# Optimization experiments

Hardware: AMD Instinct MI355X
Metric: run time of the kernel (lower is better)

## Reference

```python
import jax, jax.numpy as jnp
import numpy as np

B, T, D_IN, D, KS = 8, 2048, 64, 512, 3
N_LAYERS = 6
TOP_P = 0.25


def _causal_conv(x, w, b, dil):
    # x: [B, C_in, T], w: [C_out, C_in, K] -> [B, C_out, T]
    pad = (w.shape[-1] - 1) * dil
    y = jax.lax.conv_general_dilated(
        x, w, window_strides=(1,), padding=[(pad, 0)], rhs_dilation=(dil,),
        dimension_numbers=('NCH', 'OIH', 'NCH'))
    return y + b[None, :, None]


def setup_inputs() -> dict:
    key = jax.random.key(0)
    ks = jax.random.split(key, 20)
    s = 0.02
    inp = {
        'x': jax.random.normal(ks[0], (B, T, D_IN), jnp.float32),
        # block 0 (d_in=64 -> d_model=512, dilation 1) + 1x1 residual
        'c1w0': jax.random.normal(ks[1], (D, D_IN, KS), jnp.float32) * s,
        'c1b0': jnp.zeros((D,), jnp.float32),
        'c2w0': jax.random.normal(ks[2], (D, D, KS), jnp.float32) * s,
        'c2b0': jnp.zeros((D,), jnp.float32),
        'resw': jax.random.normal(ks[3], (D, D_IN, 1), jnp.float32) * s,
        'resb': jnp.zeros((D,), jnp.float32),
        # blocks 1..5 stacked (512 -> 512, dilations 2,4,8,16,32), identity residual
        'c1w': jax.random.normal(ks[4], (N_LAYERS - 1, D, D, KS), jnp.float32) * s,
        'c1b': jnp.zeros((N_LAYERS - 1, D), jnp.float32),
        'c2w': jax.random.normal(ks[5], (N_LAYERS - 1, D, D, KS), jnp.float32) * s,
        'c2b': jnp.zeros((N_LAYERS - 1, D), jnp.float32),
        # attention projections (torch Linear: y = x @ W.T + b, W [out,in])
        'wq': jax.random.normal(ks[6], (D, D), jnp.float32) * s,
        'bq': jnp.zeros((D,), jnp.float32),
        'wk': jax.random.normal(ks[7], (D, D), jnp.float32) * s,
        'bk': jnp.zeros((D,), jnp.float32),
        'wv': jax.random.normal(ks[8], (D, D), jnp.float32) * s,
        'bv': jnp.zeros((D,), jnp.float32),
        'wp': jax.random.normal(ks[9], (D, D), jnp.float32) * s,
        'bp': jnp.zeros((D,), jnp.float32),
    }
    return inp


def _forward(x, c1w0, c1b0, c2w0, c2b0, resw, resb, c1w, c1b, c2w, c2b,
             wq, bq, wk, bk, wv, bv, wp, bp):
    gelu = lambda t: jax.nn.gelu(t, approximate=False)
    h = jnp.swapaxes(x, 1, 2)  # [B, D_IN, T]
    # block 0 with 1x1-conv residual (d_in != d_out)
    y = gelu(_causal_conv(h, c1w0, c1b0, 1))
    y = gelu(_causal_conv(y, c2w0, c2b0, 1))
    h = y + _causal_conv(h, resw, resb, 1)
    # blocks 1..5, identity residual
    for i in range(N_LAYERS - 1):
        dil = 2 ** (i + 1)
        y = gelu(_causal_conv(h, c1w[i], c1b[i], dil))
        y = gelu(_causal_conv(y, c2w[i], c2b[i], dil))
        h = y + h
    z = jnp.swapaxes(h, 1, 2)  # [B, T, D]

    # sparse top-p attention
    q = z @ wq.T + bq
    k = z @ wk.T + bk
    v = z @ wv.T + bv
    scores = jnp.einsum('bqd,bkd->bqk', q, k) / jnp.sqrt(jnp.float32(D))
    k_keep = max(1, int(TOP_P * T))
    vals, idx = jax.lax.top_k(scores, k_keep)  # [B, T, k_keep]
    neg_inf = jnp.array(-jnp.inf, scores.dtype)
    mask = jnp.full_like(scores, neg_inf)
    b_ix = jnp.arange(B)[:, None, None]
    t_ix = jnp.arange(T)[None, :, None]
    mask = mask.at[b_ix, t_ix, idx].set(vals)
    attn = jax.nn.softmax(mask, axis=-1)
    attn_out = jnp.einsum('bqk,bkd->bqd', attn, v)[:, -1, :]  # [B, D]

    return (z[:, -1, :] + attn_out) @ wp.T + bp


def reference(x, c1w0, c1b0, c2w0, c2b0, resw, resb, c1w, c1b, c2w, c2b,
              wq, bq, wk, bk, wv, bv, wp, bp):
    return _forward(x, c1w0, c1b0, c2w0, c2b0, resw, resb, c1w, c1b, c2w, c2b,
                    wq, bq, wk, bk, wv, bv, wp, bp)
```

## Files before the change

kernel.cpp:

```cpp
#include <hip/hip_runtime.h>
#include <hip/hip_bf16.h>
#include <math.h>

#define B_ 8
#define T_ 2048
#define PT_ 2112
#define DIN_ 64
#define D_ 512

typedef __attribute__((ext_vector_type(8))) short bf16x8;
typedef __attribute__((ext_vector_type(4))) float f32x4;

#define HROW(b, t) (((size_t)(b) * PT_ + 64 + (t)) * D_)

__device__ __forceinline__ float gelu_f(float x) {
    return 0.5f * x * (1.0f + erff(x * 0.70710678118654752440f));
}
__device__ __forceinline__ float bfu2f(unsigned short u) {
    union { float f; unsigned int i; } v; v.i = ((unsigned int)u) << 16; return v.f;
}
__device__ __forceinline__ unsigned short f2bf(float f) {
    unsigned int x = __float_as_uint(f);
    return (unsigned short)((x + 0x7FFFu + ((x >> 16) & 1u)) >> 16);
}
__device__ __forceinline__ void gload_lds16(const void* g, void* l) {
    __builtin_amdgcn_global_load_lds(
        (const __attribute__((address_space(1))) void*)g,
        (__attribute__((address_space(3))) void*)l, 16, 0, 0);
}

__global__ __launch_bounds__(256) void k_zeropad(unsigned short* xb,
                                                 unsigned short* bufA,
                                                 unsigned short* bufB) {
    const int NX = B_ * 64 * DIN_;
    const int NA = B_ * 64 * D_;
    int i = blockIdx.x * 256 + threadIdx.x;
    if (i < NX) {
        const int b = i / (64 * DIN_), r = i - b * (64 * DIN_);
        xb[(size_t)b * PT_ * DIN_ + r] = 0;
        return;
    }
    i -= NX;
    if (i < NA) {
        const int b = i / (64 * D_), r = i - b * (64 * D_);
        bufA[(size_t)b * PT_ * D_ + r] = 0;
        return;
    }
    i -= NA;
    if (i < NA) {
        const int b = i / (64 * D_), r = i - b * (64 * D_);
        bufB[(size_t)b * PT_ * D_ + r] = 0;
    }
}

__global__ __launch_bounds__(256) void k_xcvt(const float* __restrict__ x,
                                              unsigned short* __restrict__ xb, int n) {
    const int i = blockIdx.x * 256 + threadIdx.x;
    if (i >= n) return;
    const int b = i / (T_ * DIN_);
    const int r = i - b * (T_ * DIN_);
    xb[((size_t)b * PT_ + 64) * DIN_ + r] = f2bf(x[i]);
}

__global__ __launch_bounds__(256) void k_wcvt(const float* __restrict__ src,
                                              unsigned short* __restrict__ dst,
                                              int C_in, int KS) {
    const int n = 512 * C_in * KS;
    const size_t base = (size_t)blockIdx.y * n;
    for (int i = blockIdx.x * 256 + threadIdx.x; i < n; i += gridDim.x * 256) {
        const int ci = i % C_in;
        const int r = i / C_in;
        const int co = r & 511;
        const int tap = r >> 9;
        dst[base + i] = f2bf(src[base + ((size_t)co * C_in + ci) * KS + tap]);
    }
}

template <int KS, int MODE>
__global__ __launch_bounds__(256, 2) void k_conv_mfma(const unsigned short* __restrict__ X,
                                                      const unsigned short* __restrict__ Wt,
                                                      const float* __restrict__ bias,
                                                      const unsigned short* R,
                                                      unsigned short* Y,
                                                      int C_in, int dil) {
    constexpr int XROWS = 192;
    constexpr int WROWS = KS * 128;
    constexpr int WSLOTS = WROWS * 8;

    const int tid = threadIdx.x;
    const int t0 = blockIdx.x * 128;
    const int co0 = blockIdx.y * 128;
    const int b = blockIdx.z;
    const int back = (KS - 1) * dil;

    __shared__ __align__(16) unsigned short sX[XROWS * 64];
    __shared__ __align__(16) unsigned short sW[WROWS * 64];

    const int lane = tid & 63;
    const int wv = tid >> 6;
    const int wco = (wv & 1) * 64;
    const int wt = (wv >> 1) * 64;
    const int tl = lane & 15;
    const int ch = lane >> 4;

    f32x4 acc[4][4] = {};

    const unsigned short* Xb = X + ((size_t)b * PT_ + 64) * C_in;

    const unsigned short* xsrc[6];
#pragma unroll
    for (int k = 0; k < 6; ++k) {
        const int i = tid + k * 256;
        const int row = i >> 3, s = i & 7;
        int tg = t0 - back + row;
        if (tg >= T_) tg = T_ - 1;
        xsrc[k] = Xb + (size_t)tg * C_in + ((s ^ (row & 7)) << 3);
    }
    const unsigned short* wsrc[WSLOTS / 256];
#pragma unroll
    for (int k = 0; k < WSLOTS / 256; ++k) {
        const int i = tid + k * 256;
        const int row = i >> 3, s = i & 7;
        const int tap = row >> 7, rco = row & 127;
        wsrc[k] = Wt + ((size_t)(tap * 512 + co0 + rco)) * C_in + ((s ^ (row & 7)) << 3);
    }

    const int NC = C_in >> 6;
    for (int c = 0; c < NC; ++c) {
        if (c) __syncthreads();
#pragma unroll
        for (int k = 0; k < 6; ++k) {
            const int i = tid + k * 256;
            gload_lds16(xsrc[k], &sX[(i & ~63) * 8]);
            xsrc[k] += 64;
        }
#pragma unroll
        for (int k = 0; k < WSLOTS / 256; ++k) {
            const int i = tid + k * 256;
            gload_lds16(wsrc[k], &sW[(i & ~63) * 8]);
            wsrc[k] += 64;
        }
        __syncthreads();

#pragma unroll
        for (int tap = 0; tap < KS; ++tap) {
            const int tapoff = tap * dil;
#pragma unroll
            for (int ks = 0; ks < 2; ++ks) {
                const int j = ks * 4 + ch;
                bf16x8 a[4], bb[4];
#pragma unroll
                for (int m = 0; m < 4; ++m) {
                    const int wr = tap * 128 + wco + m * 16 + tl;
                    a[m] = *reinterpret_cast<const bf16x8*>(
                        &sW[wr * 64 + ((j ^ (wr & 7)) << 3)]);
                }
#pragma unroll
                for (int n = 0; n < 4; ++n) {
                    const int xr = wt + n * 16 + tl + tapoff;
                    bb[n] = *reinterpret_cast<const bf16x8*>(
                        &sX[xr * 64 + ((j ^ (xr & 7)) << 3)]);
                }
#pragma unroll
                for (int m = 0; m < 4; ++m)
#pragma unroll
                    for (int n = 0; n < 4; ++n)
                        acc[m][n] = __builtin_amdgcn_mfma_f32_16x16x32_bf16(a[m], bb[n], acc[m][n], 0, 0, 0);
            }
        }
    }

#pragma unroll
    for (int m = 0; m < 4; ++m) {
        const int co = co0 + wco + m * 16 + ch * 4;
        const float4 bv4 = *reinterpret_cast<const float4*>(&bias[co]);
#pragma unroll
        for (int n = 0; n < 4; ++n) {
            const int t = t0 + wt + n * 16 + tl;
            const size_t base = HROW(b, t) + co;
            float v[4];
            v[0] = acc[m][n][0] + bv4.x;
            v[1] = acc[m][n][1] + bv4.y;
            v[2] = acc[m][n][2] + bv4.z;
            v[3] = acc[m][n][3] + bv4.w;
            if (MODE >= 1) {
#pragma unroll
                for (int r = 0; r < 4; ++r) v[r] = gelu_f(v[r]);
            }
            if (MODE == 2) {
                const uint2 rr = *reinterpret_cast<const uint2*>(&R[base]);
                v[0] += bfu2f((unsigned short)(rr.x & 0xffffu));
                v[1] += bfu2f((unsigned short)(rr.x >> 16));
                v[2] += bfu2f((unsigned short)(rr.y & 0xffffu));
                v[3] += bfu2f((unsigned short)(rr.y >> 16));
            }
            uint2 o;
            o.x = (unsigned int)f2bf(v[0]) | ((unsigned int)f2bf(v[1]) << 16);
            o.y = (unsigned int)f2bf(v[2]) | ((unsigned int)f2bf(v[3]) << 16);
            *reinterpret_cast<uint2*>(&Y[base]) = o;
        }
    }
}

__global__ __launch_bounds__(256) void k_q(const unsigned short* __restrict__ h,
                                           const float* __restrict__ wq,
                                           const float* __restrict__ bq,
                                           float* __restrict__ q) {
    __shared__ float zs[B_ * D_];
    const int tid = threadIdx.x;
    for (int i = tid; i < B_ * D_; i += 256) {
        const int b = i >> 9, c = i & 511;
        zs[i] = bfu2f(h[HROW(b, T_ - 1) + c]);
    }
    __syncthreads();
    const int wvi = tid >> 6, lane = tid & 63;
    const int d = blockIdx.x * 4 + wvi;
    const float* wr = wq + (size_t)d * D_ + lane * 8;
    float w8[8];
#pragma unroll
    for (int j = 0; j < 8; ++j) w8[j] = wr[j];
    float acc[B_];
#pragma unroll
    for (int b = 0; b < B_; ++b) {
        float a = 0.0f;
#pragma unroll
        for (int j = 0; j < 8; ++j) a += w8[j] * zs[b * D_ + lane * 8 + j];
        acc[b] = a;
    }
#pragma unroll
    for (int off = 32; off; off >>= 1) {
#pragma unroll
        for (int b = 0; b < B_; ++b) acc[b] += __shfl_xor(acc[b], off);
    }
    if (lane == 0) {
#pragma unroll
        for (int b = 0; b < B_; ++b) q[b * D_ + d] = acc[b] + bq[d];
    }
}

__global__ __launch_bounds__(512) void k_qk(const float* __restrict__ q,
                                            const float* __restrict__ wk,
                                            const float* __restrict__ bk,
                                            float* __restrict__ qkvec,
                                            float* __restrict__ qbk) {
    const int b = blockIdx.y, dc = blockIdx.x;
    const int tid = threadIdx.x;
    __shared__ float qs[64];
    if (tid < 64) qs[tid] = q[b * D_ + dc * 64 + tid];
    __syncthreads();
    float acc = 0.0f;
    const float* wbase = wk + (size_t)(dc * 64) * D_ + tid;
#pragma unroll 8
    for (int d = 0; d < 64; ++d) acc += qs[d] * wbase[(size_t)d * D_];
    atomicAdd(&qkvec[b * D_ + tid], acc);
    if (tid < 64) {
        float p = qs[tid] * bk[dc * 64 + tid];
#pragma unroll
        for (int off = 32; off; off >>= 1) p += __shfl_xor(p, off);
        if (tid == 0) atomicAdd(&qbk[b], p);
    }
}

__global__ __launch_bounds__(256) void k_scores(const unsigned short* __restrict__ h,
                                                const float* __restrict__ qkvec,
                                                const float* __restrict__ qbk,
                                                float* __restrict__ scores) {
    const int b = blockIdx.y;
    const int tid = threadIdx.x;
    __shared__ float qs[D_];
    qs[tid] = qkvec[b * D_ + tid];
    qs[tid + 256] = qkvec[b * D_ + tid + 256];
    __syncthreads();
    const int wvi = tid >> 6, lane = tid & 63;
    const int t = blockIdx.x * 4 + wvi;
    const uint4 v = *reinterpret_cast<const uint4*>(h + HROW(b, t) + lane * 8);
    const unsigned int w[4] = {v.x, v.y, v.z, v.w};
    float acc = 0.0f;
#pragma unroll
    for (int j = 0; j < 4; ++j) {
        acc += bfu2f((unsigned short)(w[j] & 0xffffu)) * qs[lane * 8 + 2 * j];
        acc += bfu2f((unsigned short)(w[j] >> 16)) * qs[lane * 8 + 2 * j + 1];
    }
    for (int off = 32; off; off >>= 1) acc += __shfl_down(acc, off);
    if (lane == 0) scores[b * T_ + t] = (acc + qbk[b]) * 0.04419417382415922f;
}

__global__ __launch_bounds__(1024) void k_topk(const float* __restrict__ scores,
                                               float* __restrict__ wts) {
    const int b = blockIdx.x;
    __shared__ float s[T_];
    __shared__ float v[T_];
    __shared__ float red[16];
    __shared__ float denom_s;
    for (int i = threadIdx.x; i < T_; i += 1024) {
        const float x = scores[b * T_ + i];
        s[i] = x; v[i] = x;
    }
    __syncthreads();
    for (unsigned kk = 2; kk <= T_; kk <<= 1) {
        for (unsigned j = kk >> 1; j > 0; j >>= 1) {
            for (unsigned i = threadIdx.x; i < T_; i += 1024) {
                const unsigned ixj = i ^ j;
                if (ixj > i) {
                    const float a = v[i], c2 = v[ixj];
                    const bool asc = ((i & kk) == 0);
                    if ((a > c2) == asc) { v[i] = c2; v[ixj] = a; }
                }
            }
            __syncthreads();
        }
    }
    const float thr = v[T_ - 512];
    const float mx = v[T_ - 1];
    float part = 0.0f;
    for (int i = threadIdx.x; i < T_; i += 1024) {
        const float x = s[i];
        if (x >= thr) part += expf(x - mx);
    }
    for (int off = 32; off; off >>= 1) part += __shfl_down(part, off);
    const int lane = threadIdx.x & 63, wv_ = threadIdx.x >> 6;
    if (lane == 0) red[wv_] = part;
    __syncthreads();
    if (threadIdx.x == 0) {
        float d = 0.0f;
        for (int i = 0; i < 16; ++i) d += red[i];
        denom_s = d;
    }
    __syncthreads();
    const float inv = 1.0f / denom_s;
    for (int i = threadIdx.x; i < T_; i += 1024) {
        const float x = s[i];
        wts[b * T_ + i] = (x >= thr) ? expf(x - mx) * inv : 0.0f;
    }
}

__global__ __launch_bounds__(256) void k_zv(const unsigned short* __restrict__ h,
                                            const float* __restrict__ wts,
                                            float* __restrict__ zvb) {
    const int b = blockIdx.y;
    const int t0 = blockIdx.x * 256;
    const int tid = threadIdx.x;
    float a0 = 0.0f, a1 = 0.0f;
    for (int t = t0; t < t0 + 256; ++t) {
        const float w = wts[b * T_ + t];
        if (w != 0.0f) {
            const unsigned int v = *reinterpret_cast<const unsigned int*>(
                h + HROW(b, t) + tid * 2);
            a0 += w * bfu2f((unsigned short)(v & 0xffffu));
            a1 += w * bfu2f((unsigned short)(v >> 16));
        }
    }
    atomicAdd(&zvb[b * D_ + tid * 2], a0);
    atomicAdd(&zvb[b * D_ + tid * 2 + 1], a1);
}

__global__ __launch_bounds__(256) void k_u(const unsigned short* __restrict__ h,
                                           const float* __restrict__ zvb,
                                           const float* __restrict__ wv,
                                           const float* __restrict__ bv,
                                           float* __restrict__ u) {
    __shared__ float zs[B_ * D_];
    const int tid = threadIdx.x;
    for (int i = tid; i < B_ * D_; i += 256) zs[i] = zvb[i];
    __syncthreads();
    const int wvi = tid >> 6, lane = tid & 63;
    const int e = blockIdx.x * 4 + wvi;
    const float* wr = wv + (size_t)e * D_ + lane * 8;
    float w8[8];
#pragma unroll
    for (int j = 0; j < 8; ++j) w8[j] = wr[j];
    float acc[B_];
#pragma unroll
    for (int b = 0; b < B_; ++b) {
        float a = 0.0f;
#pragma unroll
        for (int j = 0; j < 8; ++j) a += w8[j] * zs[b * D_ + lane * 8 + j];
        acc[b] = a;
    }
#pragma unroll
    for (int off = 32; off; off >>= 1) {
#pragma unroll
        for (int b = 0; b < B_; ++b) acc[b] += __shfl_xor(acc[b], off);
    }
    if (lane == 0) {
#pragma unroll
        for (int b = 0; b < B_; ++b)
            u[b * D_ + e] = acc[b] + bv[e] + bfu2f(h[HROW(b, T_ - 1) + e]);
    }
}

__global__ __launch_bounds__(256) void k_out(const float* __restrict__ u,
                                             const float* __restrict__ wp,
                                             const float* __restrict__ bp,
                                             float* __restrict__ out) {
    __shared__ float us[B_ * D_];
    const int tid = threadIdx.x;
    for (int i = tid; i < B_ * D_; i += 256) us[i] = u[i];
    __syncthreads();
    const int wvi = tid >> 6, lane = tid & 63;
    const int d = blockIdx.x * 4 + wvi;
    const float* wr = wp + (size_t)d * D_ + lane * 8;
    float w8[8];
#pragma unroll
    for (int j = 0; j < 8; ++j) w8[j] = wr[j];
    float acc[B_];
#pragma unroll
    for (int b = 0; b < B_; ++b) {
        float a = 0.0f;
#pragma unroll
        for (int j = 0; j < 8; ++j) a += w8[j] * us[b * D_ + lane * 8 + j];
        acc[b] = a;
    }
#pragma unroll
    for (int off = 32; off; off >>= 1) {
#pragma unroll
        for (int b = 0; b < B_; ++b) acc[b] += __shfl_xor(acc[b], off);
    }
    if (lane == 0) {
#pragma unroll
        for (int b = 0; b < B_; ++b) out[b * D_ + d] = acc[b] + bp[d];
    }
}

extern "C" void kernel_launch(void* const* d_in, const int* in_sizes, int n_in,
                              void* d_out, int out_size, void* d_ws, size_t ws_size,
                              hipStream_t stream) {
    const float* x    = (const float*)d_in[0];
    const float* c1w0 = (const float*)d_in[1];
    const float* c1b0 = (const float*)d_in[2];
    const float* c2w0 = (const float*)d_in[3];
    const float* c2b0 = (const float*)d_in[4];
    const float* resw = (const float*)d_in[5];
    const float* resb = (const float*)d_in[6];
    const float* c1w  = (const float*)d_in[7];
    const float* c1b  = (const float*)d_in[8];
    const float* c2w  = (const float*)d_in[9];
    const float* c2b  = (const float*)d_in[10];
    const float* wq   = (const float*)d_in[11];
    const float* bq   = (const float*)d_in[12];
    const float* wk   = (const float*)d_in[13];
    const float* bk   = (const float*)d_in[14];
    const float* wvp  = (const float*)d_in[15];
    const float* bv   = (const float*)d_in[16];
    const float* wp   = (const float*)d_in[17];
    const float* bp   = (const float*)d_in[18];
    float* out = (float*)d_out;

    unsigned short* ws16 = (unsigned short*)d_ws;
    unsigned short* xb   = ws16;
    unsigned short* bufA = xb + (size_t)B_ * PT_ * DIN_;
    unsigned short* bufB = bufA + (size_t)B_ * PT_ * D_;
    unsigned short* wRes = bufB + (size_t)B_ * PT_ * D_;
    unsigned short* wC10 = wRes + 512 * 64;
    unsigned short* wC20 = wC10 + 3 * 512 * 64;
    unsigned short* wC1  = wC20 + 3 * 512 * 512;
    unsigned short* wC2  = wC1 + (size_t)5 * 3 * 512 * 512;
    float* fws  = (float*)(wC2 + (size_t)5 * 3 * 512 * 512);
    float* qv    = fws;
    float* qkvec = qv + B_ * D_;
    float* qbk   = qkvec + B_ * D_;
    float* zvb   = qbk + 8;
    float* uacc  = zvb + B_ * D_;
    float* sc    = uacc + B_ * D_;
    float* wts   = sc + B_ * T_;

    k_zeropad<<<dim3((B_ * 64 * (DIN_ + 2 * D_) + 255) / 256), 256, 0, stream>>>(xb, bufA, bufB);
    k_xcvt<<<dim3((B_ * T_ * DIN_ + 255) / 256), 256, 0, stream>>>(x, xb, B_ * T_ * DIN_);
    k_wcvt<<<dim3(128, 1), 256, 0, stream>>>(resw, wRes, DIN_, 1);
    k_wcvt<<<dim3(384, 1), 256, 0, stream>>>(c1w0, wC10, DIN_, 3);
    k_wcvt<<<dim3(768, 1), 256, 0, stream>>>(c2w0, wC20, D_, 3);
    k_wcvt<<<dim3(768, 5), 256, 0, stream>>>(c1w, wC1, D_, 3);
    k_wcvt<<<dim3(768, 5), 256, 0, stream>>>(c2w, wC2, D_, 3);
    hipMemsetAsync(qkvec, 0, (2 * B_ * D_ + 8) * sizeof(float), stream);

    const dim3 cgrid(T_ / 128, D_ / 128, B_);
    k_conv_mfma<1, 0><<<cgrid, 256, 0, stream>>>(xb, wRes, resb, nullptr, bufA, DIN_, 1);
    k_conv_mfma<3, 1><<<cgrid, 256, 0, stream>>>(xb, wC10, c1b0, nullptr, bufB, DIN_, 1);
    k_conv_mfma<3, 2><<<cgrid, 256, 0, stream>>>(bufB, wC20, c2b0, bufA, bufA, D_, 1);
    for (int i = 0; i < 5; ++i) {
        const int dil = 2 << i;
        k_conv_mfma<3, 1><<<cgrid, 256, 0, stream>>>(bufA, wC1 + (size_t)i * 3 * 512 * 512,
                                                     c1b + i * D_, nullptr, bufB, D_, dil);
        k_conv_mfma<3, 2><<<cgrid, 256, 0, stream>>>(bufB, wC2 + (size_t)i * 3 * 512 * 512,
                                                     c2b + i * D_, bufA, bufA, D_, dil);
    }

    k_q<<<128, 256, 0, stream>>>(bufA, wq, bq, qv);
    k_qk<<<dim3(8, 8), 512, 0, stream>>>(qv, wk, bk, qkvec, qbk);
    k_scores<<<dim3(T_ / 4, B_), 256, 0, stream>>>(bufA, qkvec, qbk, sc);
    k_topk<<<B_, 1024, 0, stream>>>(sc, wts);
    k_zv<<<dim3(T_ / 256, B_), 256, 0, stream>>>(bufA, wts, zvb);
    k_u<<<128, 256, 0, stream>>>(bufA, zvb, wvp, bv, uacc);
    k_out<<<128, 256, 0, stream>>>(uacc, wp, bp, out);
}
```

Before: 475.0 us.

## Software-pipeline conv MFMA kernel with double-buffered per-tap weight and input staging

Restructures the conv main loop into per-tap phases with double-buffered LDS for both inputs and weights. Global-to-LDS loads for the next tap or channel chunk are issued before the current MFMAs, with explicit vmcnt/lgkmcnt waits and barriers. MFMA blocks are wrapped in s_setprio to favour compute issue. The aim is to hide global load latency behind matrix math, at the cost of more barriers and fragile hand-tuned wait counts.

Result: slower. 491.3 us (+3.4%).

```diff
diff --git a/kernel.cpp b/kernel.cpp
--- a/kernel.cpp
+++ b/kernel.cpp
@@ -83,18 +83,14 @@
                                                       const unsigned short* R,
                                                       unsigned short* Y,
                                                       int C_in, int dil) {
-    constexpr int XROWS = 192;
-    constexpr int WROWS = KS * 128;
-    constexpr int WSLOTS = WROWS * 8;
-
     const int tid = threadIdx.x;
     const int t0 = blockIdx.x * 128;
     const int co0 = blockIdx.y * 128;
     const int b = blockIdx.z;
     const int back = (KS - 1) * dil;
 
-    __shared__ __align__(16) unsigned short sX[XROWS * 64];
-    __shared__ __align__(16) unsigned short sW[WROWS * 64];
+    __shared__ __align__(16) unsigned short sX[2][192 * 64];
+    __shared__ __align__(16) unsigned short sW[2][128 * 64];
 
     const int lane = tid & 63;
     const int wv = tid >> 6;
@@ -116,57 +112,124 @@
         if (tg >= T_) tg = T_ - 1;
         xsrc[k] = Xb + (size_t)tg * C_in + ((s ^ (row & 7)) << 3);
     }
-    const unsigned short* wsrc[WSLOTS / 256];
-#pragma unroll
-    for (int k = 0; k < WSLOTS / 256; ++k) {
+    const unsigned short* wsrc[4];
+#pragma unroll
+    for (int k = 0; k < 4; ++k) {
         const int i = tid + k * 256;
         const int row = i >> 3, s = i & 7;
-        const int tap = row >> 7, rco = row & 127;
-        wsrc[k] = Wt + ((size_t)(tap * 512 + co0 + rco)) * C_in + ((s ^ (row & 7)) << 3);
-    }
-
-    const int NC = C_in >> 6;
-    for (int c = 0; c < NC; ++c) {
-        if (c) __syncthreads();
+        wsrc[k] = Wt + (size_t)(co0 + row) * C_in + ((s ^ (row & 7)) << 3);
+    }
+    const size_t tapstride = (size_t)512 * C_in;
+
+    auto stageX = [&](int c) {
+        unsigned short* dst = sX[c & 1];
 #pragma unroll
         for (int k = 0; k < 6; ++k) {
             const int i = tid + k * 256;
-            gload_lds16(xsrc[k], &sX[(i & ~63) * 8]);
-            xsrc[k] += 64;
-        }
-#pragma unroll
-        for (int k = 0; k < WSLOTS / 256; ++k) {
+            gload_lds16(xsrc[k] + c * 64, &dst[(i & ~63) * 8]);
+        }
+    };
+    auto stageW = [&](int c, int tap, int buf) {
+        unsigned short* dst = sW[buf];
+#pragma unroll
+        for (int k = 0; k < 4; ++k) {
             const int i = tid + k * 256;
-            gload_lds16(wsrc[k], &sW[(i & ~63) * 8]);
-            wsrc[k] += 64;
-        }
+            gload_lds16(wsrc[k] + (size_t)tap * tapstride + c * 64, &dst[(i & ~63) * 8]);
+        }
+    };
+    auto phase_reads = [&](int pp, int cb, int tap, bf16x8 (&a)[2][4], bf16x8 (&bb)[2][4]) {
+        const unsigned short* bW = sW[pp];
+        const unsigned short* bX = sX[cb];
+        const int tapoff = tap * dil;
+#pragma unroll
+        for (int ks = 0; ks < 2; ++ks) {
+            const int j = ks * 4 + ch;
+#pragma unroll
+            for (int m = 0; m < 4; ++m) {
+                const int wr = wco + m * 16 + tl;
+                a[ks][m] = *reinterpret_cast<const bf16x8*>(&bW[wr * 64 + ((j ^ (wr & 7)) << 3)]);
+            }
+#pragma unroll
+            for (int n = 0; n < 4; ++n) {
+                const int xr = wt + n * 16 + tl + tapoff;
+                bb[ks][n] = *reinterpret_cast<const bf16x8*>(&bX[xr * 64 + ((j ^ (xr & 7)) << 3)]);
+            }
+        }
+    };
+    auto domfma = [&](bf16x8 (&a)[2][4], bf16x8 (&bb)[2][4]) {
+        __builtin_amdgcn_s_setprio(1);
+#pragma unroll
+        for (int ks = 0; ks < 2; ++ks)
+#pragma unroll
+            for (int m = 0; m < 4; ++m)
+#pragma unroll
+                for (int n = 0; n < 4; ++n)
+                    acc[m][n] = __builtin_amdgcn_mfma_f32_16x16x32_bf16(a[ks][m], bb[ks][n], acc[m][n], 0, 0, 0);
+        __builtin_amdgcn_s_setprio(0);
+    };
+
+    if constexpr (KS == 1) {
+        stageX(0);
+        stageW(0, 0, 0);
         __syncthreads();
-
-#pragma unroll
-        for (int tap = 0; tap < KS; ++tap) {
-            const int tapoff = tap * dil;
-#pragma unroll
-            for (int ks = 0; ks < 2; ++ks) {
-                const int j = ks * 4 + ch;
-                bf16x8 a[4], bb[4];
-#pragma unroll
-                for (int m = 0; m < 4; ++m) {
-                    const int wr = tap * 128 + wco + m * 16 + tl;
-                    a[m] = *reinterpret_cast<const bf16x8*>(
-                        &sW[wr * 64 + ((j ^ (wr & 7)) << 3)]);
-                }
-#pragma unroll
-                for (int n = 0; n < 4; ++n) {
-                    const int xr = wt + n * 16 + tl + tapoff;
-                    bb[n] = *reinterpret_cast<const bf16x8*>(
-                        &sX[xr * 64 + ((j ^ (xr & 7)) << 3)]);
-                }
-#pragma unroll
-                for (int m = 0; m < 4; ++m)
-#pragma unroll
-                    for (int n = 0; n < 4; ++n)
-                        acc[m][n] = __builtin_amdgcn_mfma_f32_16x16x32_bf16(a[m], bb[n], acc[m][n], 0, 0, 0);
-            }
+        bf16x8 a[2][4], bb[2][4];
+        phase_reads(0, 0, 0, a, bb);
+        domfma(a, bb);
+    } else {
+        const int NC = C_in >> 6;
+        const int NPH = NC * 3;
+        stageX(0);
+        stageW(0, 0, 0);
+        stageW(0, 1, 1);
+        asm volatile("s_waitcnt vmcnt(4)" ::: "memory");
+        __builtin_amdgcn_sched_barrier(0);
+        __builtin_amdgcn_s_barrier();
+
+        int c = 0, t = 0;
+        for (int ph = 0; ph + 3 < NPH; ++ph) {
+            bf16x8 a[2][4], bb[2][4];
+            phase_reads(ph & 1, c & 1, t, a, bb);
+            asm volatile("s_waitcnt lgkmcnt(0)" ::: "memory");
+            __builtin_amdgcn_sched_barrier(0);
+            __builtin_amdgcn_s_barrier();
+            int t2 = t + 2, c2 = c;
+            if (t2 >= 3) { t2 -= 3; ++c2; }
+            stageW(c2, t2, ph & 1);
+            if (t == 0) stageX(c + 1);
+            domfma(a, bb);
+            if (t < 2) { asm volatile("s_waitcnt vmcnt(10)" ::: "memory"); }
+            else       { asm volatile("s_waitcnt vmcnt(4)"  ::: "memory"); }
+            __builtin_amdgcn_sched_barrier(0);
+            __builtin_amdgcn_s_barrier();
+            if (++t == 3) { t = 0; ++c; }
+        }
+        {
+            bf16x8 a[2][4], bb[2][4];
+            phase_reads((NPH - 3) & 1, (NC - 1) & 1, 0, a, bb);
+            asm volatile("s_waitcnt lgkmcnt(0)" ::: "memory");
+            __builtin_amdgcn_sched_barrier(0);
+            __builtin_amdgcn_s_barrier();
+            stageW(NC - 1, 2, (NPH - 3) & 1);
+            domfma(a, bb);
+            asm volatile("s_waitcnt vmcnt(4)" ::: "memory");
+            __builtin_amdgcn_sched_barrier(0);
+            __builtin_amdgcn_s_barrier();
+        }
+        {
+            bf16x8 a[2][4], bb[2][4];
+            phase_reads((NPH - 2) & 1, (NC - 1) & 1, 1, a, bb);
+            asm volatile("s_waitcnt lgkmcnt(0)" ::: "memory");
+            __builtin_amdgcn_sched_barrier(0);
+            __builtin_amdgcn_s_barrier();
+            domfma(a, bb);
+            asm volatile("s_waitcnt vmcnt(0)" ::: "memory");
+            __builtin_amdgcn_sched_barrier(0);
+            __builtin_amdgcn_s_barrier();
+        }
+        {
+            bf16x8 a[2][4], bb[2][4];
+            phase_reads((NPH - 1) & 1, (NC - 1) & 1, 2, a, bb);
+            domfma(a, bb);
         }
     }
 
```

## Widen conv tile to 256 time steps and halve channel chunk to 32

Applied to the files above, without the earlier changes.

The MFMA conv kernel now has each block cover 256 time steps by 128 output channels. Each of the four warps owns 64 time steps across all 128 output channels, so it holds an 8x4 accumulator grid and reuses each loaded B fragment across more MFMAs. The input-channel chunk per LDS stage drops from 64 to 32, which shrinks shared memory and lowers the relative cost of the dilation halo. In exchange the grid has half as many blocks, there are twice as many sync/load rounds per block, and the larger accumulator raises register pressure.

New measurement: 671.3 us. 1.41x slower.

```diff
diff --git a/kernel.cpp b/kernel.cpp
--- a/kernel.cpp
+++ b/kernel.cpp
@@ -83,96 +83,86 @@
                                                       const unsigned short* R,
                                                       unsigned short* Y,
                                                       int C_in, int dil) {
-    constexpr int XROWS = 192;
-    constexpr int WROWS = KS * 128;
-    constexpr int WSLOTS = WROWS * 8;
-
-    const int tid = threadIdx.x;
-    const int t0 = blockIdx.x * 128;
+    const int tid = threadIdx.x;
+    const int t0 = blockIdx.x * 256;
     const int co0 = blockIdx.y * 128;
     const int b = blockIdx.z;
     const int back = (KS - 1) * dil;
-
-    __shared__ __align__(16) unsigned short sX[XROWS * 64];
-    __shared__ __align__(16) unsigned short sW[WROWS * 64];
+    const int nx = (256 + back) * 4;
+
+    __shared__ __align__(16) unsigned short sX[320 * 32];
+    __shared__ __align__(16) unsigned short sW[KS * 128 * 32];
 
     const int lane = tid & 63;
     const int wv = tid >> 6;
-    const int wco = (wv & 1) * 64;
-    const int wt = (wv >> 1) * 64;
+    const int wt = wv * 64;
     const int tl = lane & 15;
     const int ch = lane >> 4;
 
-    f32x4 acc[4][4] = {};
+    f32x4 acc[8][4] = {};
 
     const unsigned short* Xb = X + ((size_t)b * PT_ + 64) * C_in;
 
-    const unsigned short* xsrc[6];
-#pragma unroll
-    for (int k = 0; k < 6; ++k) {
+    const unsigned short* xsrc[5];
+#pragma unroll
+    for (int k = 0; k < 5; ++k) {
         const int i = tid + k * 256;
-        const int row = i >> 3, s = i & 7;
+        const int row = i >> 2, s = i & 3;
         int tg = t0 - back + row;
         if (tg >= T_) tg = T_ - 1;
-        xsrc[k] = Xb + (size_t)tg * C_in + ((s ^ (row & 7)) << 3);
-    }
-    const unsigned short* wsrc[WSLOTS / 256];
-#pragma unroll
-    for (int k = 0; k < WSLOTS / 256; ++k) {
+        xsrc[k] = Xb + (size_t)tg * C_in + ((s ^ (row & 3)) << 3);
+    }
+    const unsigned short* wsrc[KS * 2];
+#pragma unroll
+    for (int k = 0; k < KS * 2; ++k) {
         const int i = tid + k * 256;
-        const int row = i >> 3, s = i & 7;
+        const int row = i >> 2, s = i & 3;
         const int tap = row >> 7, rco = row & 127;
-        wsrc[k] = Wt + ((size_t)(tap * 512 + co0 + rco)) * C_in + ((s ^ (row & 7)) << 3);
-    }
-
-    const int NC = C_in >> 6;
+        wsrc[k] = Wt + ((size_t)(tap * 512 + co0 + rco)) * C_in + ((s ^ (row & 3)) << 3);
+    }
+
+    const int NC = C_in >> 5;
     for (int c = 0; c < NC; ++c) {
         if (c) __syncthreads();
 #pragma unroll
-        for (int k = 0; k < 6; ++k) {
+        for (int k = 0; k < 5; ++k) {
             const int i = tid + k * 256;
-            gload_lds16(xsrc[k], &sX[(i & ~63) * 8]);
-            xsrc[k] += 64;
-        }
-#pragma unroll
-        for (int k = 0; k < WSLOTS / 256; ++k) {
+            if (i < nx) gload_lds16(xsrc[k] + c * 32, &sX[(i & ~63) * 8]);
+        }
+#pragma unroll
+        for (int k = 0; k < KS * 2; ++k) {
             const int i = tid + k * 256;
-            gload_lds16(wsrc[k], &sW[(i & ~63) * 8]);
-            wsrc[k] += 64;
+            gload_lds16(wsrc[k] + c * 32, &sW[(i & ~63) * 8]);
         }
         __syncthreads();
 
 #pragma unroll
         for (int tap = 0; tap < KS; ++tap) {
             const int tapoff = tap * dil;
-#pragma unroll
-            for (int ks = 0; ks < 2; ++ks) {
-                const int j = ks * 4 + ch;
-                bf16x8 a[4], bb[4];
-#pragma unroll
-                for (int m = 0; m < 4; ++m) {
-                    const int wr = tap * 128 + wco + m * 16 + tl;
-                    a[m] = *reinterpret_cast<const bf16x8*>(
-                        &sW[wr * 64 + ((j ^ (wr & 7)) << 3)]);
-                }
-#pragma unroll
-                for (int n = 0; n < 4; ++n) {
-                    const int xr = wt + n * 16 + tl + tapoff;
-                    bb[n] = *reinterpret_cast<const bf16x8*>(
-                        &sX[xr * 64 + ((j ^ (xr & 7)) << 3)]);
-                }
-#pragma unroll
-                for (int m = 0; m < 4; ++m)
-#pragma unroll
-                    for (int n = 0; n < 4; ++n)
-                        acc[m][n] = __builtin_amdgcn_mfma_f32_16x16x32_bf16(a[m], bb[n], acc[m][n], 0, 0, 0);
+            bf16x8 a[8], bb[4];
+#pragma unroll
+            for (int m = 0; m < 8; ++m) {
+                const int wr = tap * 128 + m * 16 + tl;
+                a[m] = *reinterpret_cast<const bf16x8*>(
+                    &sW[wr * 32 + ((ch ^ (wr & 3)) << 3)]);
             }
-        }
-    }
-
-#pragma unroll
-    for (int m = 0; m < 4; ++m) {
-        const int co = co0 + wco + m * 16 + ch * 4;
+#pragma unroll
+            for (int n = 0; n < 4; ++n) {
+                const int xr = wt + n * 16 + tl + tapoff;
+                bb[n] = *reinterpret_cast<const bf16x8*>(
+                    &sX[xr * 32 + ((ch ^ (xr & 3)) << 3)]);
+            }
+#pragma unroll
+            for (int m = 0; m < 8; ++m)
+#pragma unroll
+                for (int n = 0; n < 4; ++n)
+                    acc[m][n] = __builtin_amdgcn_mfma_f32_16x16x32_bf16(a[m], bb[n], acc[m][n], 0, 0, 0);
+        }
+    }
+
+#pragma unroll
+    for (int m = 0; m < 8; ++m) {
+        const int co = co0 + m * 16 + ch * 4;
         const float4 bv4 = *reinterpret_cast<const float4*>(&bias[co]);
 #pragma unroll
         for (int n = 0; n < 4; ++n) {
@@ -473,7 +463,7 @@
     k_wcvt<<<dim3(768, 5), 256, 0, stream>>>(c2w, wC2, D_, 3);
     hipMemsetAsync(qkvec, 0, (2 * B_ * D_ + 8) * sizeof(float), stream);
 
-    const dim3 cgrid(T_ / 128, D_ / 128, B_);
+    const dim3 cgrid(T_ / 256, D_ / 128, B_);
     k_conv_mfma<1, 0><<<cgrid, 256, 0, stream>>>(xb, wRes, resb, nullptr, bufA, DIN_, 1);
     k_conv_mfma<3, 1><<<cgrid, 256, 0, stream>>>(xb, wC10, c1b0, nullptr, bufB, DIN_, 1);
     k_conv_mfma<3, 2><<<cgrid, 256, 0, stream>>>(bufB, wC20, c2b0, bufA, bufA, D_, 1);
```

## Double-buffer conv LDS tiles with 32-channel chunks to overlap loads and MFMA

Applied to the files above, without the earlier changes.

Restructures the MFMA conv kernel's channel loop to use two LDS buffers of 32-channel chunks. The next chunk's global-to-LDS loads are issued right after the barrier so they overlap the current chunk's MFMAs, with one barrier per iteration instead of two. It also skips loading unneeded X halo rows for small dilations and raises wave priority around the MFMA bursts. In exchange there are twice as many loop iterations with less work each, and the vmcnt(0) wait still stalls each iteration on the previous prefetch.

Result: slower. 510.2 us (+7.4%).

```diff
diff --git a/kernel.cpp b/kernel.cpp
--- a/kernel.cpp
+++ b/kernel.cpp
@@ -83,18 +83,15 @@
                                                       const unsigned short* R,
                                                       unsigned short* Y,
                                                       int C_in, int dil) {
-    constexpr int XROWS = 192;
-    constexpr int WROWS = KS * 128;
-    constexpr int WSLOTS = WROWS * 8;
-
     const int tid = threadIdx.x;
     const int t0 = blockIdx.x * 128;
     const int co0 = blockIdx.y * 128;
     const int b = blockIdx.z;
     const int back = (KS - 1) * dil;
-
-    __shared__ __align__(16) unsigned short sX[XROWS * 64];
-    __shared__ __align__(16) unsigned short sW[WROWS * 64];
+    const int nx = (128 + back) * 4;
+
+    __shared__ __align__(16) unsigned short sX[2][192 * 32];
+    __shared__ __align__(16) unsigned short sW[2][KS * 128 * 32];
 
     const int lane = tid & 63;
     const int wv = tid >> 6;
@@ -107,66 +104,73 @@
 
     const unsigned short* Xb = X + ((size_t)b * PT_ + 64) * C_in;
 
-    const unsigned short* xsrc[6];
-#pragma unroll
-    for (int k = 0; k < 6; ++k) {
+    const unsigned short* xsrc[3];
+#pragma unroll
+    for (int k = 0; k < 3; ++k) {
         const int i = tid + k * 256;
-        const int row = i >> 3, s = i & 7;
+        const int row = i >> 2, s = i & 3;
         int tg = t0 - back + row;
         if (tg >= T_) tg = T_ - 1;
-        xsrc[k] = Xb + (size_t)tg * C_in + ((s ^ (row & 7)) << 3);
-    }
-    const unsigned short* wsrc[WSLOTS / 256];
-#pragma unroll
-    for (int k = 0; k < WSLOTS / 256; ++k) {
+        xsrc[k] = Xb + (size_t)tg * C_in + ((s ^ ((row >> 1) & 3)) << 3);
+    }
+    const unsigned short* wsrc[KS * 2];
+#pragma unroll
+    for (int k = 0; k < KS * 2; ++k) {
         const int i = tid + k * 256;
-        const int row = i >> 3, s = i & 7;
+        const int row = i >> 2, s = i & 3;
         const int tap = row >> 7, rco = row & 127;
-        wsrc[k] = Wt + ((size_t)(tap * 512 + co0 + rco)) * C_in + ((s ^ (row & 7)) << 3);
-    }
-
-    const int NC = C_in >> 6;
+        wsrc[k] = Wt + ((size_t)(tap * 512 + co0 + rco)) * C_in + ((s ^ ((row >> 1) & 3)) << 3);
+    }
+
+    auto stage = [&](int c) {
+        unsigned short* dX = sX[c & 1];
+        unsigned short* dW = sW[c & 1];
+#pragma unroll
+        for (int k = 0; k < 3; ++k) {
+            const int i = tid + k * 256;
+            if (i < nx) gload_lds16(xsrc[k] + c * 32, &dX[(i & ~63) * 8]);
+        }
+#pragma unroll
+        for (int k = 0; k < KS * 2; ++k) {
+            const int i = tid + k * 256;
+            gload_lds16(wsrc[k] + c * 32, &dW[(i & ~63) * 8]);
+        }
+    };
+
+    const int NC = C_in >> 5;
+    stage(0);
     for (int c = 0; c < NC; ++c) {
-        if (c) __syncthreads();
-#pragma unroll
-        for (int k = 0; k < 6; ++k) {
-            const int i = tid + k * 256;
-            gload_lds16(xsrc[k], &sX[(i & ~63) * 8]);
-            xsrc[k] += 64;
-        }
-#pragma unroll
-        for (int k = 0; k < WSLOTS / 256; ++k) {
-            const int i = tid + k * 256;
-            gload_lds16(wsrc[k], &sW[(i & ~63) * 8]);
-            wsrc[k] += 64;
-        }
-        __syncthreads();
-
+        asm volatile("s_waitcnt vmcnt(0)" ::: "memory");
+        __builtin_amdgcn_sched_barrier(0);
+        __builtin_amdgcn_s_barrier();
+        __builtin_amdgcn_sched_barrier(0);
+        if (c + 1 < NC) stage(c + 1);
+
+        const unsigned short* bX = sX[c & 1];
+        const unsigned short* bW = sW[c & 1];
 #pragma unroll
         for (int tap = 0; tap < KS; ++tap) {
             const int tapoff = tap * dil;
-#pragma unroll
-            for (int ks = 0; ks < 2; ++ks) {
-                const int j = ks * 4 + ch;
-                bf16x8 a[4], bb[4];
-#pragma unroll
-                for (int m = 0; m < 4; ++m) {
-                    const int wr = tap * 128 + wco + m * 16 + tl;
-                    a[m] = *reinterpret_cast<const bf16x8*>(
-                        &sW[wr * 64 + ((j ^ (wr & 7)) << 3)]);
-                }
-#pragma unroll
-                for (int n = 0; n < 4; ++n) {
-                    const int xr = wt + n * 16 + tl + tapoff;
-                    bb[n] = *reinterpret_cast<const bf16x8*>(
-                        &sX[xr * 64 + ((j ^ (xr & 7)) << 3)]);
-                }
-#pragma unroll
-                for (int m = 0; m < 4; ++m)
-#pragma unroll
-                    for (int n = 0; n < 4; ++n)
-                        acc[m][n] = __builtin_amdgcn_mfma_f32_16x16x32_bf16(a[m], bb[n], acc[m][n], 0, 0, 0);
+            bf16x8 a[4], bb[4];
+#pragma unroll
+            for (int m = 0; m < 4; ++m) {
+                const int wr = tap * 128 + wco + m * 16 + tl;
+                a[m] = *reinterpret_cast<const bf16x8*>(
+                    &bW[wr * 32 + ((ch ^ ((wr >> 1) & 3)) << 3)]);
             }
+#pragma unroll
+            for (int n = 0; n < 4; ++n) {
+                const int xr = wt + n * 16 + tl + tapoff;
+                bb[n] = *reinterpret_cast<const bf16x8*>(
+                    &bX[xr * 32 + ((ch ^ ((xr >> 1) & 3)) << 3)]);
+            }
+            __builtin_amdgcn_s_setprio(1);
+#pragma unroll
+            for (int m = 0; m < 4; ++m)
+#pragma unroll
+                for (int n = 0; n < 4; ++n)
+                    acc[m][n] = __builtin_amdgcn_mfma_f32_16x16x32_bf16(a[m], bb[n], acc[m][n], 0, 0, 0);
+            __builtin_amdgcn_s_setprio(0);
         }
     }
 
```
